# Optimization experiments

Hardware: AMD Instinct MI355X
Metric: run time of the kernel (lower is better)

The kernel has to match this reference:

```python
import jax, jax.numpy as jnp
import numpy as np

DEPTH = 256
HEADS = 8
K = 128          # kernel_size == attended axis length (height)
DH = DEPTH // HEADS  # 32
EPS = 1e-5


def _bn(x, gamma, beta, axes):
    # training-mode batch norm (biased variance), per-channel on axis 1
    mean = jnp.mean(x, axis=axes, keepdims=True)
    var = jnp.var(x, axis=axes, keepdims=True)
    shape = [1] * x.ndim
    shape[1] = x.shape[1]
    g = gamma.reshape(shape)
    b = beta.reshape(shape)
    return (x - mean) * jax.lax.rsqrt(var + EPS) * g + b


def setup_inputs() -> dict:
    key = jax.random.key(0)
    ks = jax.random.split(key, 3)
    x = jax.random.normal(ks[0], (2, DEPTH, K, K), dtype=jnp.float32)
    w_kqv = jax.random.normal(ks[1], (2 * DEPTH, DEPTH), dtype=jnp.float32) * 0.05
    rel_encoding = jax.random.normal(ks[2], (2 * DH, 2 * K - 1), dtype=jnp.float32)
    return {
        "x": x,
        "w_kqv": w_kqv,
        "kqv_gamma": jnp.ones((2 * DEPTH,), jnp.float32),
        "kqv_beta": jnp.zeros((2 * DEPTH,), jnp.float32),
        "logits_gamma": jnp.ones((3 * HEADS,), jnp.float32),
        "logits_beta": jnp.zeros((3 * HEADS,), jnp.float32),
        "rel_encoding": rel_encoding,
    }


def reference(x, w_kqv, kqv_gamma, kqv_beta, logits_gamma, logits_beta, rel_encoding):
    B, C, H, W = x.shape  # height_dim=True path
    # (B,C,H,W) -> (B,W,C,H) -> (B*W, C, H)
    xf = jnp.transpose(x, (0, 3, 1, 2)).reshape(B * W, C, H)
    # 1x1 conv == channel matmul
    kqv = jnp.einsum('oc,bch->boh', w_kqv, xf)  # (BW, 2*depth, H)
    kqv = _bn(kqv, kqv_gamma, kqv_beta, axes=(0, 2))
    kqv = kqv.reshape(B * W, HEADS, 2 * DH, H)
    k = kqv[:, :, : DH // 2]            # (BW, h, dh/2, H)
    q = kqv[:, :, DH // 2: DH]          # (BW, h, dh/2, H)
    v = kqv[:, :, DH:]                  # (BW, h, dh,   H)

    # relative position gather: (2*dh, 2K-1) -> (2*dh, K, K)
    idx = (jnp.arange(K)[None, :] - jnp.arange(K)[:, None] + K - 1).reshape(-1)
    rel = rel_encoding[:, idx].reshape(2 * DH, K, K)
    q_enc = rel[: DH // 2]
    k_enc = rel[DH // 2: DH]
    v_enc = rel[DH:]

    qk = jnp.einsum('bhdx,bhdy->bhxy', q, k)
    qr = jnp.einsum('bhdx,dxy->bhxy', q, q_enc)
    kr = jnp.swapaxes(jnp.einsum('bhdx,dxy->bhxy', k, k_enc), 2, 3)
    logits = jnp.concatenate([qk, qr, kr], axis=1)  # (BW, 3*h, K, K)
    logits = _bn(logits, logits_gamma, logits_beta, axes=(0, 2, 3))
    logits = logits.reshape(B * W, 3, HEADS, H, H).sum(axis=1)
    weights = jax.nn.softmax(logits, axis=3)  # (BW, h, K, K)

    attn = jnp.einsum('bhxy,bhdy->bhdx', weights, v)         # (BW, h, dh, H)
    attn_enc = jnp.einsum('bhxy,dxy->bhdx', weights, v_enc)  # (BW, h, dh, H)
    out = (attn + attn_enc).reshape(B, W, DEPTH, H)  # cat+reshape+sum(dim=-2) == add
    out = jnp.transpose(out, (0, 2, 3, 1))  # (B, depth, H, W)
    return out
```

## Files before the change

kernel.cpp:

```cpp
#include <hip/hip_runtime.h>
#include <hip/hip_bf16.h>

#define H 128
#define NB 256
#define OC 512
#define CIN 256
#define NN 16384
#define EPS 1e-5f

typedef __attribute__((ext_vector_type(4))) float f32x4;
typedef __attribute__((ext_vector_type(8))) short bf16x8;
typedef unsigned short u16x8 __attribute__((ext_vector_type(8)));

__device__ __forceinline__ float bf2f(unsigned short u){
    return __uint_as_float(((unsigned int)u) << 16);
}
__device__ __forceinline__ unsigned short f2bf(float f){
    unsigned int x = __float_as_uint(f);
    return (unsigned short)((x + 0x7fffu + ((x >> 16) & 1u)) >> 16);
}
__device__ __forceinline__ float ldin(const void* p, size_t i, bool f32){
    return f32 ? ((const float*)p)[i] : bf2f(((const unsigned short*)p)[i]);
}
__device__ __forceinline__ short ld_bf16(const void* p, size_t i, bool f32){
    if (f32) return (short)f2bf(((const float*)p)[i]);
    return ((const short*)p)[i];
}
__device__ __forceinline__ bool probe_f32(const void* gamma_ones){
    return *(const unsigned int*)gamma_ones == 0x3F800000u;
}

template<bool F32>
__device__ __forceinline__ void gemm_body(const void* __restrict__ w,
                                          const void* __restrict__ x,
                                          unsigned short* __restrict__ c1,
                                          short (*As)[128][40], short (*Bs)[64][40])
{
    const int m0 = blockIdx.x * 128;
    const int n0 = blockIdx.y * 64;
    const int b0 = blockIdx.z;
    const int t  = threadIdx.x;
    const int lane = t & 63, wv = t >> 6;
    const int wm = wv & 1, wn = wv >> 1;
    const int lm = lane & 15, quad = lane >> 4;
    const size_t xb = (size_t)b0 * CIN * NN;
    const int am = t >> 1, ak = (t & 1) * 16;
    const int bn = t & 63, bk = (t >> 6) * 8;

    float4 pa[4]; float pb[8];
    u16x8 qa[2]; unsigned short qb[8];

    auto load_tile = [&](int k0){
        if constexpr (F32){
            const float* wp = (const float*)w + (size_t)(m0+am)*CIN + k0 + ak;
            #pragma unroll
            for (int q=0;q<4;q++) pa[q] = *(const float4*)(wp + 4*q);
            const float* xp = (const float*)x + xb + (size_t)(k0+bk)*NN + n0 + bn;
            #pragma unroll
            for (int i=0;i<8;i++) pb[i] = xp[(size_t)i*NN];
        } else {
            const unsigned short* wp = (const unsigned short*)w + (size_t)(m0+am)*CIN + k0 + ak;
            qa[0] = *(const u16x8*)wp; qa[1] = *(const u16x8*)(wp+8);
            const unsigned short* xp = (const unsigned short*)x + xb + (size_t)(k0+bk)*NN + n0 + bn;
            #pragma unroll
            for (int i=0;i<8;i++) qb[i] = xp[(size_t)i*NN];
        }
    };
    auto store_tile = [&](int buf){
        if constexpr (F32){
            short ta[16];
            #pragma unroll
            for (int q=0;q<4;q++){
                ta[4*q+0]=(short)f2bf(pa[q].x); ta[4*q+1]=(short)f2bf(pa[q].y);
                ta[4*q+2]=(short)f2bf(pa[q].z); ta[4*q+3]=(short)f2bf(pa[q].w);
            }
            *(bf16x8*)&As[buf][am][ak]   = *(bf16x8*)&ta[0];
            *(bf16x8*)&As[buf][am][ak+8] = *(bf16x8*)&ta[8];
            #pragma unroll
            for (int i=0;i<8;i++) Bs[buf][bn][bk+i] = (short)f2bf(pb[i]);
        } else {
            *(u16x8*)&As[buf][am][ak]   = qa[0];
            *(u16x8*)&As[buf][am][ak+8] = qa[1];
            #pragma unroll
            for (int i=0;i<8;i++) Bs[buf][bn][bk+i] = (short)qb[i];
        }
    };

    f32x4 acc[4][2];
    #pragma unroll
    for (int i=0;i<4;i++){ acc[i][0]=(f32x4){0,0,0,0}; acc[i][1]=(f32x4){0,0,0,0}; }

    load_tile(0); store_tile(0); __syncthreads();
    for (int kk=0; kk<8; ++kk){
        const int cur = kk & 1;
        if (kk < 7) load_tile((kk+1)*32);
        bf16x8 af[4], bfB[2];
        #pragma unroll
        for (int i=0;i<4;i++) af[i]  = *(const bf16x8*)&As[cur][wm*64 + i*16 + lm][quad*8];
        #pragma unroll
        for (int j=0;j<2;j++) bfB[j] = *(const bf16x8*)&Bs[cur][wn*32 + j*16 + lm][quad*8];
        #pragma unroll
        for (int i=0;i<4;i++)
            #pragma unroll
            for (int j=0;j<2;j++)
                acc[i][j] = __builtin_amdgcn_mfma_f32_16x16x32_bf16(af[i], bfB[j], acc[i][j], 0,0,0);
        if (kk < 7) store_tile(cur ^ 1);
        __syncthreads();
    }
    #pragma unroll
    for (int i=0;i<4;i++){
        #pragma unroll
        for (int j=0;j<2;j++){
            int n = n0 + wn*32 + j*16 + lm;
            #pragma unroll
            for (int r=0;r<4;r++){
                int m = m0 + wm*64 + i*16 + quad*4 + r;
                c1[((size_t)b0*OC + m)*NN + n] = f2bf(acc[i][j][r]);
            }
        }
    }
}

__global__ __launch_bounds__(256) void k_gemm(const void* __restrict__ w,
                                              const void* __restrict__ x,
                                              unsigned short* __restrict__ c1,
                                              const void* __restrict__ probe)
{
    __shared__ short As[2][128][40];
    __shared__ short Bs[2][64][40];
    if (probe_f32(probe)) gemm_body<true >(w, x, c1, As, Bs);
    else                  gemm_body<false>(w, x, c1, As, Bs);
}

__global__ __launch_bounds__(256) void k_bn_transpose(const unsigned short* __restrict__ c1,
        unsigned short* __restrict__ kqvt,
        const void* __restrict__ gamma, const void* __restrict__ beta)
{
    __shared__ float T[128][129];
    __shared__ float red[8];
    __shared__ float sc_sh[2];
    const bool f32 = probe_f32(gamma);
    const int o = blockIdx.x;
    const int t = threadIdx.x;
    const int lane = t & 63, wv = t >> 6;
    const unsigned short* r0 = c1 + (size_t)o*NN;
    const unsigned short* r1 = c1 + ((size_t)OC + o)*NN;
    const u16x8* r08 = (const u16x8*)r0;
    const u16x8* r18 = (const u16x8*)r1;
    float s=0.f, ss=0.f;
    #pragma unroll
    for (int i=0;i<8;i++){
        u16x8 a = r08[t + i*256];
        u16x8 b = r18[t + i*256];
        #pragma unroll
        for (int e=0;e<8;e++){
            float va = bf2f(a[e]); s += va; ss = fmaf(va,va,ss);
            float vb = bf2f(b[e]); s += vb; ss = fmaf(vb,vb,ss);
        }
    }
    #pragma unroll
    for (int off=1; off<64; off<<=1){ s += __shfl_xor(s,off); ss += __shfl_xor(ss,off); }
    if (lane==0){ red[wv*2] = s; red[wv*2+1] = ss; }
    __syncthreads();
    if (t==0){
        float st=0.f, sq=0.f;
        for (int i=0;i<4;i++){ st += red[i*2]; sq += red[i*2+1]; }
        float mean = st * (1.f/32768.f);
        float var  = sq * (1.f/32768.f) - mean*mean;
        float scale = ldin(gamma, o, f32) * rsqrtf(var + EPS);
        sc_sh[0] = scale;
        sc_sh[1] = ldin(beta, o, f32) - mean*scale;
    }
    __syncthreads();
    const float scale = sc_sh[0], shift = sc_sh[1];
    for (int b0=0;b0<2;b0++){
        const unsigned short* r = b0 ? r1 : r0;
        for (int i=0;i<64;i++){
            int idx = t + i*256;
            int h = idx >> 7, ww = idx & 127;
            T[ww][h] = fmaf(bf2f(r[idx]), scale, shift);
        }
        __syncthreads();
        for (int i=0;i<64;i++){
            int idx = t + i*256;
            int ww = idx >> 7, h = idx & 127;
            kqvt[(((size_t)(b0*128 + ww))*OC + o)*H + h] = f2bf(T[ww][h]);
        }
        __syncthreads();
    }
}

__global__ __launch_bounds__(256) void k_logit_stats(const unsigned short* __restrict__ kqvt,
        const void* __restrict__ relenc, float* __restrict__ stats,
        const void* __restrict__ probe)
{
    __shared__ short QA[128][40];
    __shared__ short KA[128][40];
    __shared__ short EQ[256][24];
    __shared__ short EK[256][24];
    __shared__ alignas(16) short ZED[16];
    __shared__ float wr[4][6];
    const bool f32 = probe_f32(probe);
    const int b = blockIdx.x >> 3, head = blockIdx.x & 7;
    const int t = threadIdx.x;
    const int lane = t & 63, wv = t >> 6;
    const int lm = lane & 15, quad = lane >> 4;
    const unsigned short* base = kqvt + ((size_t)b*OC + head*64)*H;
    {
        int dd = t & 15, xg = (t >> 4) * 8;
        u16x8 kv = *(const u16x8*)&base[dd*H + xg];
        u16x8 qv = *(const u16x8*)&base[(16+dd)*H + xg];
        #pragma unroll
        for (int e=0;e<8;e++){
            QA[xg+e][dd] = (short)qv[e]; QA[xg+e][16+dd] = 0;
            KA[xg+e][dd] = (short)kv[e]; KA[xg+e][16+dd] = 0;
        }
    }
    {
        int c = t & 15, jb = (t >> 4) * 16;
        short tq[16], tk[16];
        #pragma unroll
        for (int i=0;i<16;i++){
            int j = jb + i;
            tq[i] = (j<255) ? ld_bf16(relenc, (size_t)c*255 + j, f32) : (short)0;
            tk[i] = (j<255) ? ld_bf16(relenc, (size_t)(16+c)*255 + j, f32) : (short)0;
        }
        #pragma unroll
        for (int i=0;i<16;i++){ EQ[jb+i][c] = tq[i]; EK[jb+i][c] = tk[i]; }
    }
    if (t < 16) ZED[t] = 0;
    __syncthreads();

    float s_qk=0,s_qr=0,s_kr=0,q_qk=0,q_qr=0,q_kr=0;
    #pragma unroll
    for (int u=0;u<2;u++){
        const int mt = 2*wv + u;
        bf16x8 aq = *(const bf16x8*)&QA[mt*16 + lm][quad*8];
        bf16x8 ak = *(const bf16x8*)&KA[mt*16 + lm][quad*8];
        #pragma unroll
        for (int yt=0; yt<8; ++yt){
            bf16x8 bk = *(const bf16x8*)&KA[yt*16 + lm][quad*8];
            f32x4 c = __builtin_amdgcn_mfma_f32_16x16x32_bf16(aq, bk,
                        (f32x4){0.f,0.f,0.f,0.f}, 0,0,0);
            #pragma unroll
            for (int r=0;r<4;r++){ s_qk += c[r]; q_qk = fmaf(c[r],c[r],q_qk); }
        }
        for (int jt=0; jt<16; ++jt){
            int sdiag = mt + jt;
            if (sdiag < 7 || sdiag > 15) continue;
            const short* pq = (quad < 2) ? &EQ[jt*16 + lm][quad*8] : &ZED[0];
            const short* pk = (quad < 2) ? &EK[jt*16 + lm][quad*8] : &ZED[0];
            f32x4 cq = __builtin_amdgcn_mfma_f32_16x16x32_bf16(aq, *(const bf16x8*)pq,
                         (f32x4){0.f,0.f,0.f,0.f}, 0,0,0);
            f32x4 ck = __builtin_amdgcn_mfma_f32_16x16x32_bf16(ak, *(const bf16x8*)pk,
                         (f32x4){0.f,0.f,0.f,0.f}, 0,0,0);
            int j = jt*16 + lm;
            #pragma unroll
            for (int r=0;r<4;r++){
                int xy = mt*16 + quad*4 + r;
                int o1 = xy + j - 127;
                if ((unsigned)o1 < 128u){
                    s_qr += cq[r]; q_qr = fmaf(cq[r],cq[r],q_qr);
                    s_kr += ck[r]; q_kr = fmaf(ck[r],ck[r],q_kr);
                }
            }
        }
    }
    #pragma unroll
    for (int off=1; off<64; off<<=1){
        s_qk += __shfl_xor(s_qk,off); s_qr += __shfl_xor(s_qr,off); s_kr += __shfl_xor(s_kr,off);
        q_qk += __shfl_xor(q_qk,off); q_qr += __shfl_xor(q_qr,off); q_kr += __shfl_xor(q_kr,off);
    }
    if (lane==0){ wr[wv][0]=s_qk; wr[wv][1]=s_qr; wr[wv][2]=s_kr;
                  wr[wv][3]=q_qk; wr[wv][4]=q_qr; wr[wv][5]=q_kr; }
    __syncthreads();
    if (t==0){
        float a0=0,a1=0,a2=0,b0_=0,b1=0,b2=0;
        for (int i=0;i<4;i++){ a0+=wr[i][0]; a1+=wr[i][1]; a2+=wr[i][2];
                               b0_+=wr[i][3]; b1+=wr[i][4]; b2+=wr[i][5]; }
        atomicAdd(&stats[head],      a0);
        atomicAdd(&stats[8+head],    a1);
        atomicAdd(&stats[16+head],   a2);
        atomicAdd(&stats[24+head],   b0_);
        atomicAdd(&stats[24+8+head], b1);
        atomicAdd(&stats[24+16+head],b2);
    }
}

__global__ void k_scales(const float* __restrict__ stats, float* __restrict__ scales,
                         const void* __restrict__ gamma_l, const void* __restrict__ probe)
{
    const bool f32 = probe_f32(probe);
    int t = threadIdx.x;
    if (t < 24){
        const float inv_cnt = 1.f/4194304.f;
        float mean = stats[t]*inv_cnt;
        float var  = stats[24+t]*inv_cnt - mean*mean;
        scales[t] = ldin(gamma_l, t, f32) * rsqrtf(var + EPS);
    }
}

struct SA {
    short QA[128][40];
    short KA[128][40];
    short EQ[256][24];
    short EK[256][24];
};
struct SV {
    short Vs[32][136];
    short Evs[32][264];
};
union SU { SA a; SV v; };

__global__ __launch_bounds__(256) void k_attn(const unsigned short* __restrict__ kqvt,
        const void* __restrict__ relenc,
        const float* __restrict__ scales,
        void* __restrict__ outp,
        const void* __restrict__ probe)
{
    __shared__ SU smu;
    __shared__ short RW[128][136];
    __shared__ alignas(16) short ZED[16];
    const bool f32 = probe_f32(probe);
    const int blk = blockIdx.x;
    const int b = blk >> 3, head = blk & 7;
    const int b0 = b >> 7, w = b & 127;
    const int t = threadIdx.x;
    const int lane = t & 63, wv = t >> 6;
    const int lm = lane & 15, quad = lane >> 4;
    const unsigned short* base = kqvt + ((size_t)b*OC + head*64)*H;
    const float s0 = scales[head], s1 = scales[8+head], s2 = scales[16+head];

    {
        int dd = t & 15, xg = (t >> 4) * 8;
        u16x8 kv = *(const u16x8*)&base[dd*H + xg];
        u16x8 qv = *(const u16x8*)&base[(16+dd)*H + xg];
        #pragma unroll
        for (int e=0;e<8;e++){
            smu.a.QA[xg+e][dd] = (short)qv[e]; smu.a.QA[xg+e][16+dd] = 0;
            smu.a.KA[xg+e][dd] = (short)kv[e]; smu.a.KA[xg+e][16+dd] = 0;
        }
    }
    {
        int c = t & 15, jb = (t >> 4) * 16;
        short tq[16], tk[16];
        #pragma unroll
        for (int i=0;i<16;i++){
            int j = jb + i;
            float vq = (j<255) ? ldin(relenc, (size_t)c*255 + j, f32) : 0.f;
            float vk = (j<255) ? ldin(relenc, (size_t)(16+c)*255 + j, f32) : 0.f;
            tq[i] = (short)f2bf(s1*vq); tk[i] = (short)f2bf(s2*vk);
        }
        #pragma unroll
        for (int i=0;i<16;i++){ smu.a.EQ[jb+i][c] = tq[i]; smu.a.EK[jb+i][c] = tk[i]; }
    }
    if (t < 16) ZED[t] = 0;
    __syncthreads();

    f32x4 qacc[2][8];
    bf16x8 aq[2], akk[2];
    #pragma unroll
    for (int u=0;u<2;u++){
        const int mt = 2*wv + u;
        aq[u]  = *(const bf16x8*)&smu.a.QA[mt*16 + lm][quad*8];
        akk[u] = *(const bf16x8*)&smu.a.KA[mt*16 + lm][quad*8];
        #pragma unroll
        for (int yt=0; yt<8; ++yt){
            bf16x8 bk = *(const bf16x8*)&smu.a.KA[yt*16 + lm][quad*8];
            qacc[u][yt] = __builtin_amdgcn_mfma_f32_16x16x32_bf16(aq[u], bk,
                            (f32x4){0.f,0.f,0.f,0.f}, 0,0,0);
        }
        for (int jt=0; jt<16; ++jt){
            int sdiag = mt + jt;
            if (sdiag < 7 || sdiag > 15) continue;
            const short* pq = (quad < 2) ? &smu.a.EQ[jt*16 + lm][quad*8] : &ZED[0];
            f32x4 cq = __builtin_amdgcn_mfma_f32_16x16x32_bf16(aq[u], *(const bf16x8*)pq,
                         (f32x4){0.f,0.f,0.f,0.f}, 0,0,0);
            int j = jt*16 + lm;
            #pragma unroll
            for (int r=0;r<4;r++){
                int x = mt*16 + quad*4 + r;
                int y = x + j - 127;
                if ((unsigned)y < 128u) RW[x][y] = (short)f2bf(cq[r]);
            }
        }
    }
    __syncthreads();

    #pragma unroll
    for (int u=0;u<2;u++){
        const int mt = 2*wv + u;
        for (int jt=0; jt<16; ++jt){
            int sdiag = mt + jt;
            if (sdiag < 7 || sdiag > 15) continue;
            const short* pk = (quad < 2) ? &smu.a.EK[jt*16 + lm][quad*8] : &ZED[0];
            f32x4 ck = __builtin_amdgcn_mfma_f32_16x16x32_bf16(akk[u], *(const bf16x8*)pk,
                         (f32x4){0.f,0.f,0.f,0.f}, 0,0,0);
            int j = jt*16 + lm;
            #pragma unroll
            for (int r=0;r<4;r++){
                int y = mt*16 + quad*4 + r;
                int x = y + j - 127;
                if ((unsigned)x < 128u){
                    float cur = bf2f((unsigned short)RW[x][y]);
                    RW[x][y] = (short)f2bf(cur + ck[r]);
                }
            }
        }
    }
    __syncthreads();

    {
        int dd = t & 31, yg = (t >> 5) * 16;
        u16x8 v0 = *(const u16x8*)&base[(32+dd)*H + yg];
        u16x8 v1 = *(const u16x8*)&base[(32+dd)*H + yg + 8];
        *(u16x8*)&smu.v.Vs[dd][yg]   = v0;
        *(u16x8*)&smu.v.Vs[dd][yg+8] = v1;
    }
    {
        int d = t & 31, jb = (t >> 5) * 32;
        short tv[32];
        #pragma unroll
        for (int i=0;i<32;i++){
            int j = jb + i;
            tv[i] = (j < 255) ? ld_bf16(relenc, (size_t)(32+d)*255 + j, f32) : (short)0;
        }
        #pragma unroll
        for (int i=0;i<32;i+=8)
            *(u16x8*)&smu.v.Evs[d][jb+i] = *(u16x8*)&tv[i];
        if ((t >> 5) == 7)
            *(u16x8*)&smu.v.Evs[d][256] = (u16x8){0,0,0,0,0,0,0,0};
    }
    #pragma unroll
    for (int u=0;u<2;u++){
        const int mt = 2*wv + u;
        #pragma unroll
        for (int r=0;r<4;r++){
            const int x = mt*16 + quad*4 + r;
            float v[8]; float mx = -1e30f;
            #pragma unroll
            for (int yt=0; yt<8; ++yt){
                v[yt] = fmaf(s0, qacc[u][yt][r], bf2f((unsigned short)RW[x][yt*16 + lm]));
                mx = fmaxf(mx, v[yt]);
            }
            mx = fmaxf(mx, __shfl_xor(mx,1));
            mx = fmaxf(mx, __shfl_xor(mx,2));
            mx = fmaxf(mx, __shfl_xor(mx,4));
            mx = fmaxf(mx, __shfl_xor(mx,8));
            float sum = 0.f;
            #pragma unroll
            for (int yt=0; yt<8; ++yt){ v[yt] = __expf(v[yt]-mx); sum += v[yt]; }
            sum += __shfl_xor(sum,1);
            sum += __shfl_xor(sum,2);
            sum += __shfl_xor(sum,4);
            sum += __shfl_xor(sum,8);
            float inv = 1.f/sum;
            #pragma unroll
            for (int yt=0; yt<8; ++yt)
                RW[x][yt*16 + lm] = (short)f2bf(v[yt]*inv);
        }
    }
    __syncthreads();

    f32x4 o[2][2];
    #pragma unroll
    for (int u=0;u<2;u++){ o[u][0]=(f32x4){0,0,0,0}; o[u][1]=(f32x4){0,0,0,0}; }
    #pragma unroll
    for (int kt=0; kt<4; ++kt){
        bf16x8 bv0 = *(const bf16x8*)&smu.v.Vs[lm][kt*32 + quad*8];
        bf16x8 bv1 = *(const bf16x8*)&smu.v.Vs[16+lm][kt*32 + quad*8];
        #pragma unroll
        for (int u=0;u<2;u++){
            bf16x8 aw = *(const bf16x8*)&RW[(2*wv+u)*16 + lm][kt*32 + quad*8];
            o[u][0] = __builtin_amdgcn_mfma_f32_16x16x32_bf16(aw, bv0, o[u][0], 0,0,0);
            o[u][1] = __builtin_amdgcn_mfma_f32_16x16x32_bf16(aw, bv1, o[u][1], 0,0,0);
        }
    }
    for (int kt=0; kt<8; ++kt){
        bf16x8 be0 = *(const bf16x8*)&smu.v.Evs[lm][kt*32 + quad*8];
        bf16x8 be1 = *(const bf16x8*)&smu.v.Evs[16+lm][kt*32 + quad*8];
        #pragma unroll
        for (int u=0;u<2;u++){
            const int mt = 2*wv + u;
            int lo = mt*16 + kt*32 - 127;
            if (lo > 127 || lo + 46 < 0) continue;
            int xg = mt*16 + lm;
            int y0 = xg + kt*32 + quad*8 - 127;
            short g[8];
            #pragma unroll
            for (int jj=0;jj<8;jj++){
                int y = y0 + jj;
                g[jj] = ((unsigned)y < 128u) ? RW[xg][y] : (short)0;
            }
            bf16x8 ag = *(bf16x8*)g;
            o[u][0] = __builtin_amdgcn_mfma_f32_16x16x32_bf16(ag, be0, o[u][0], 0,0,0);
            o[u][1] = __builtin_amdgcn_mfma_f32_16x16x32_bf16(ag, be1, o[u][1], 0,0,0);
        }
    }
    #pragma unroll
    for (int u=0;u<2;u++){
        #pragma unroll
        for (int nt=0; nt<2; ++nt){
            int d = nt*16 + lm;
            size_t cb = ((size_t)(b0*256 + head*32 + d))*16384 + (size_t)w;
            #pragma unroll
            for (int r=0;r<4;r++){
                int x = (2*wv+u)*16 + quad*4 + r;
                if (f32) ((float*)outp)[cb + (size_t)x*128] = o[u][nt][r];
                else ((unsigned short*)outp)[cb + (size_t)x*128] = f2bf(o[u][nt][r]);
            }
        }
    }
}

extern "C" void kernel_launch(void* const* d_in, const int* in_sizes, int n_in,
                              void* d_out, int out_size, void* d_ws, size_t ws_size,
                              hipStream_t stream)
{
    (void)in_sizes; (void)n_in; (void)out_size;
    const void* x      = d_in[0];
    const void* w_kqv  = d_in[1];
    const void* kqv_g  = d_in[2];
    const void* kqv_b  = d_in[3];
    const void* log_g  = d_in[4];
    const void* relenc = d_in[6];

    if (ws_size < (size_t)64*1024*1024) return;
    unsigned short* C1   = (unsigned short*)d_ws;
    unsigned short* KQVT = C1 + 16777216;
    float* STATS  = (float*)d_ws;
    float* SCALES = STATS + 48;

    dim3 g1(OC/128, NN/64, 2);
    k_gemm<<<g1, 256, 0, stream>>>(w_kqv, x, C1, kqv_g);
    k_bn_transpose<<<512, 256, 0, stream>>>(C1, KQVT, kqv_g, kqv_b);
    hipMemsetAsync(STATS, 0, 48*sizeof(float), stream);
    k_logit_stats<<<2048, 256, 0, stream>>>(KQVT, relenc, STATS, kqv_g);
    k_scales<<<1, 64, 0, stream>>>(STATS, SCALES, log_g, kqv_g);
    k_attn<<<2048, 256, 0, stream>>>(KQVT, relenc, SCALES, d_out, kqv_g);
}
```

Before: 383.8 us.

## Fuse BN statistics into GEMM epilogue and amortize rel-encoding loads in logit stats

```diff
diff --git a/kernel.cpp b/kernel.cpp
--- a/kernel.cpp
+++ b/kernel.cpp
@@ -34,6 +34,7 @@
 __device__ __forceinline__ void gemm_body(const void* __restrict__ w,
                                           const void* __restrict__ x,
                                           unsigned short* __restrict__ c1,
+                                          float* __restrict__ kstats,
                                           short (*As)[128][40], short (*Bs)[64][40])
 {
     const int m0 = blockIdx.x * 128;
@@ -107,6 +108,7 @@
         if (kk < 7) store_tile(cur ^ 1);
         __syncthreads();
     }
+    float s2[4][4], ss2[4][4];
     #pragma unroll
     for (int i=0;i<4;i++){
         #pragma unroll
@@ -118,61 +120,68 @@
                 c1[((size_t)b0*OC + m)*NN + n] = f2bf(acc[i][j][r]);
             }
         }
+        #pragma unroll
+        for (int r=0;r<4;r++){
+            float a0 = acc[i][0][r], a1 = acc[i][1][r];
+            s2[i][r]  = a0 + a1;
+            ss2[i][r] = fmaf(a0,a0, a1*a1);
+        }
+    }
+    #pragma unroll
+    for (int off=1; off<16; off<<=1){
+        #pragma unroll
+        for (int i=0;i<4;i++)
+            #pragma unroll
+            for (int r=0;r<4;r++){
+                s2[i][r]  += __shfl_xor(s2[i][r],  off);
+                ss2[i][r] += __shfl_xor(ss2[i][r], off);
+            }
+    }
+    if (lm == 0){
+        #pragma unroll
+        for (int i=0;i<4;i++)
+            #pragma unroll
+            for (int r=0;r<4;r++){
+                int m = m0 + wm*64 + i*16 + quad*4 + r;
+                atomicAdd(&kstats[m],       s2[i][r]);
+                atomicAdd(&kstats[512 + m], ss2[i][r]);
+            }
     }
 }
 
 __global__ __launch_bounds__(256) void k_gemm(const void* __restrict__ w,
                                               const void* __restrict__ x,
                                               unsigned short* __restrict__ c1,
+                                              float* __restrict__ kstats,
                                               const void* __restrict__ probe)
 {
     __shared__ short As[2][128][40];
     __shared__ short Bs[2][64][40];
-    if (probe_f32(probe)) gemm_body<true >(w, x, c1, As, Bs);
-    else                  gemm_body<false>(w, x, c1, As, Bs);
+    if (probe_f32(probe)) gemm_body<true >(w, x, c1, kstats, As, Bs);
+    else                  gemm_body<false>(w, x, c1, kstats, As, Bs);
 }
 
 __global__ __launch_bounds__(256) void k_bn_transpose(const unsigned short* __restrict__ c1,
         unsigned short* __restrict__ kqvt,
-        const void* __restrict__ gamma, const void* __restrict__ beta)
+        const void* __restrict__ gamma, const void* __restrict__ beta,
+        const float* __restrict__ kstats)
 {
     __shared__ float T[128][129];
-    __shared__ float red[8];
     __shared__ float sc_sh[2];
     const bool f32 = probe_f32(gamma);
     const int o = blockIdx.x;
     const int t = threadIdx.x;
-    const int lane = t & 63, wv = t >> 6;
-    const unsigned short* r0 = c1 + (size_t)o*NN;
-    const unsigned short* r1 = c1 + ((size_t)OC + o)*NN;
-    const u16x8* r08 = (const u16x8*)r0;
-    const u16x8* r18 = (const u16x8*)r1;
-    float s=0.f, ss=0.f;
-    #pragma unroll
-    for (int i=0;i<8;i++){
-        u16x8 a = r08[t + i*256];
-        u16x8 b = r18[t + i*256];
-        #pragma unroll
-        for (int e=0;e<8;e++){
-            float va = bf2f(a[e]); s += va; ss = fmaf(va,va,ss);
-            float vb = bf2f(b[e]); s += vb; ss = fmaf(vb,vb,ss);
-        }
-    }
-    #pragma unroll
-    for (int off=1; off<64; off<<=1){ s += __shfl_xor(s,off); ss += __shfl_xor(ss,off); }
-    if (lane==0){ red[wv*2] = s; red[wv*2+1] = ss; }
-    __syncthreads();
     if (t==0){
-        float st=0.f, sq=0.f;
-        for (int i=0;i<4;i++){ st += red[i*2]; sq += red[i*2+1]; }
-        float mean = st * (1.f/32768.f);
-        float var  = sq * (1.f/32768.f) - mean*mean;
+        float mean = kstats[o] * (1.f/32768.f);
+        float var  = kstats[512+o] * (1.f/32768.f) - mean*mean;
         float scale = ldin(gamma, o, f32) * rsqrtf(var + EPS);
         sc_sh[0] = scale;
         sc_sh[1] = ldin(beta, o, f32) - mean*scale;
     }
     __syncthreads();
     const float scale = sc_sh[0], shift = sc_sh[1];
+    const unsigned short* r0 = c1 + (size_t)o*NN;
+    const unsigned short* r1 = c1 + ((size_t)OC + o)*NN;
     for (int b0=0;b0<2;b0++){
         const unsigned short* r = b0 ? r1 : r0;
         for (int i=0;i<64;i++){
@@ -201,21 +210,10 @@
     __shared__ alignas(16) short ZED[16];
     __shared__ float wr[4][6];
     const bool f32 = probe_f32(probe);
-    const int b = blockIdx.x >> 3, head = blockIdx.x & 7;
+    const int head = blockIdx.x & 7, chunk = blockIdx.x >> 3;
     const int t = threadIdx.x;
     const int lane = t & 63, wv = t >> 6;
     const int lm = lane & 15, quad = lane >> 4;
-    const unsigned short* base = kqvt + ((size_t)b*OC + head*64)*H;
-    {
-        int dd = t & 15, xg = (t >> 4) * 8;
-        u16x8 kv = *(const u16x8*)&base[dd*H + xg];
-        u16x8 qv = *(const u16x8*)&base[(16+dd)*H + xg];
-        #pragma unroll
-        for (int e=0;e<8;e++){
-            QA[xg+e][dd] = (short)qv[e]; QA[xg+e][16+dd] = 0;
-            KA[xg+e][dd] = (short)kv[e]; KA[xg+e][16+dd] = 0;
-        }
-    }
     {
         int c = t & 15, jb = (t >> 4) * 16;
         short tq[16], tk[16];
@@ -229,39 +227,54 @@
         for (int i=0;i<16;i++){ EQ[jb+i][c] = tq[i]; EK[jb+i][c] = tk[i]; }
     }
     if (t < 16) ZED[t] = 0;
-    __syncthreads();
 
     float s_qk=0,s_qr=0,s_kr=0,q_qk=0,q_qr=0,q_kr=0;
-    #pragma unroll
-    for (int u=0;u<2;u++){
-        const int mt = 2*wv + u;
-        bf16x8 aq = *(const bf16x8*)&QA[mt*16 + lm][quad*8];
-        bf16x8 ak = *(const bf16x8*)&KA[mt*16 + lm][quad*8];
-        #pragma unroll
-        for (int yt=0; yt<8; ++yt){
-            bf16x8 bk = *(const bf16x8*)&KA[yt*16 + lm][quad*8];
-            f32x4 c = __builtin_amdgcn_mfma_f32_16x16x32_bf16(aq, bk,
-                        (f32x4){0.f,0.f,0.f,0.f}, 0,0,0);
-            #pragma unroll
-            for (int r=0;r<4;r++){ s_qk += c[r]; q_qk = fmaf(c[r],c[r],q_qk); }
-        }
-        for (int jt=0; jt<16; ++jt){
-            int sdiag = mt + jt;
-            if (sdiag < 7 || sdiag > 15) continue;
-            const short* pq = (quad < 2) ? &EQ[jt*16 + lm][quad*8] : &ZED[0];
-            const short* pk = (quad < 2) ? &EK[jt*16 + lm][quad*8] : &ZED[0];
-            f32x4 cq = __builtin_amdgcn_mfma_f32_16x16x32_bf16(aq, *(const bf16x8*)pq,
-                         (f32x4){0.f,0.f,0.f,0.f}, 0,0,0);
-            f32x4 ck = __builtin_amdgcn_mfma_f32_16x16x32_bf16(ak, *(const bf16x8*)pk,
-                         (f32x4){0.f,0.f,0.f,0.f}, 0,0,0);
-            int j = jt*16 + lm;
-            #pragma unroll
-            for (int r=0;r<4;r++){
-                int xy = mt*16 + quad*4 + r;
-                int o1 = xy + j - 127;
-                if ((unsigned)o1 < 128u){
-                    s_qr += cq[r]; q_qr = fmaf(cq[r],cq[r],q_qr);
-                    s_kr += ck[r]; q_kr = fmaf(ck[r],ck[r],q_kr);
+    for (int bi=0; bi<4; ++bi){
+        const int b = chunk*4 + bi;
+        const unsigned short* base = kqvt + ((size_t)b*OC + head*64)*H;
+        __syncthreads();
+        {
+            int dd = t & 15, xg = (t >> 4) * 8;
+            u16x8 kv = *(const u16x8*)&base[dd*H + xg];
+            u16x8 qv = *(const u16x8*)&base[(16+dd)*H + xg];
+            #pragma unroll
+            for (int e=0;e<8;e++){
+                QA[xg+e][dd] = (short)qv[e]; QA[xg+e][16+dd] = 0;
+                KA[xg+e][dd] = (short)kv[e]; KA[xg+e][16+dd] = 0;
+            }
+        }
+        __syncthreads();
+        #pragma unroll
+        for (int u=0;u<2;u++){
+            const int mt = 2*wv + u;
+            bf16x8 aq = *(const bf16x8*)&QA[mt*16 + lm][quad*8];
+            bf16x8 ak = *(const bf16x8*)&KA[mt*16 + lm][quad*8];
+            #pragma unroll
+            for (int yt=0; yt<8; ++yt){
+                bf16x8 bk = *(const bf16x8*)&KA[yt*16 + lm][quad*8];
+                f32x4 c = __builtin_amdgcn_mfma_f32_16x16x32_bf16(aq, bk,
+                            (f32x4){0.f,0.f,0.f,0.f}, 0,0,0);
+                #pragma unroll
+                for (int r=0;r<4;r++){ s_qk += c[r]; q_qk = fmaf(c[r],c[r],q_qk); }
+            }
+            for (int jt=0; jt<16; ++jt){
+                int sdiag = mt + jt;
+                if (sdiag < 7 || sdiag > 15) continue;
+                const short* pq = (quad < 2) ? &EQ[jt*16 + lm][quad*8] : &ZED[0];
+                const short* pk = (quad < 2) ? &EK[jt*16 + lm][quad*8] : &ZED[0];
+                f32x4 cq = __builtin_amdgcn_mfma_f32_16x16x32_bf16(aq, *(const bf16x8*)pq,
+                             (f32x4){0.f,0.f,0.f,0.f}, 0,0,0);
+                f32x4 ck = __builtin_amdgcn_mfma_f32_16x16x32_bf16(ak, *(const bf16x8*)pk,
+                             (f32x4){0.f,0.f,0.f,0.f}, 0,0,0);
+                int j = jt*16 + lm;
+                #pragma unroll
+                for (int r=0;r<4;r++){
+                    int xy = mt*16 + quad*4 + r;
+                    int o1 = xy + j - 127;
+                    if ((unsigned)o1 < 128u){
+                        s_qr += cq[r]; q_qr = fmaf(cq[r],cq[r],q_qr);
+                        s_kr += ck[r]; q_kr = fmaf(ck[r],ck[r],q_kr);
+                    }
                 }
             }
         }
@@ -530,12 +543,14 @@
     unsigned short* KQVT = C1 + 16777216;
     float* STATS  = (float*)d_ws;
     float* SCALES = STATS + 48;
-
+    float* KSTATS = (float*)d_out;
+
+    hipMemsetAsync(KSTATS, 0, 1024*sizeof(float), stream);
     dim3 g1(OC/128, NN/64, 2);
-    k_gemm<<<g1, 256, 0, stream>>>(w_kqv, x, C1, kqv_g);
-    k_bn_transpose<<<512, 256, 0, stream>>>(C1, KQVT, kqv_g, kqv_b);
+    k_gemm<<<g1, 256, 0, stream>>>(w_kqv, x, C1, KSTATS, kqv_g);
+    k_bn_transpose<<<512, 256, 0, stream>>>(C1, KQVT, kqv_g, kqv_b, KSTATS);
     hipMemsetAsync(STATS, 0, 48*sizeof(float), stream);
-    k_logit_stats<<<2048, 256, 0, stream>>>(KQVT, relenc, STATS, kqv_g);
+    k_logit_stats<<<512, 256, 0, stream>>>(KQVT, relenc, STATS, kqv_g);
     k_scales<<<1, 64, 0, stream>>>(STATS, SCALES, log_g, kqv_g);
     k_attn<<<2048, 256, 0, stream>>>(KQVT, relenc, SCALES, d_out, kqv_g);
 }
```

Result: slower. 414.7 us (+8.0%).
